# Performance work log

Measured on AMD Instinct MI355X. Metric: run time of the kernel, lower is better.

Reference implementation:

```python
import jax, jax.numpy as jnp
import numpy as np

BS, D, N, E, L, NE = 8, 512, 2048, 8, 64, 524288


def conv1d_same(x, w, b):
    # x: [B, W, Cin], w: [K, Cin, Cout] -> [B, W, Cout], stride 1, 'same' padding
    y = jax.lax.conv_general_dilated(x, w, window_strides=(1,), padding='SAME',
                                     dimension_numbers=('NWC', 'WIO', 'NWC'))
    return y + b


def setup_inputs() -> dict:
    key = jax.random.key(0)
    ks = jax.random.split(key, 10)
    def nrm(k, shape, s=1.0):
        return jax.random.normal(k, shape, jnp.float32) * s
    return {
        'latent': nrm(ks[0], (BS, D)),
        'edge_index': jax.random.randint(ks[1], (2, NE), 0, BS * N),
        'W_dense': nrm(ks[2], (D, N), 0.05),
        'b_dense': jnp.zeros((N,), jnp.float32),
        'conv1_w': nrm(ks[3], (3, 1, E), 0.3),
        'conv1_b': jnp.zeros((E,), jnp.float32),
        'gat_Wq': nrm(ks[4], (E, E), 0.3),
        'gat_bq': jnp.zeros((E,), jnp.float32),
        'gat_Wk': nrm(ks[5], (E, E), 0.3),
        'gat_bk': jnp.zeros((E,), jnp.float32),
        'gat_Wv': nrm(ks[6], (E, E), 0.3),
        'gat_bias': jnp.zeros((E,), jnp.float32),
        'qkv_w': nrm(ks[7], (3, E, 3 * E * L), 0.1),
        'qkv_b': jnp.zeros((3 * E * L,), jnp.float32),
    }


def reference(latent, edge_index, W_dense, b_dense, conv1_w, conv1_b,
              gat_Wq, gat_bq, gat_Wk, gat_bk, gat_Wv, gat_bias, qkv_w, qkv_b):
    bs = latent.shape[0]
    # Dense -> [bs, N], expand -> Conv1D(E) -> [bs, N, E]
    skeleton = latent @ W_dense + b_dense
    skeleton = conv1d_same(skeleton[..., None], conv1_w, conv1_b)
    # concat(unstack, axis=0) == reshape to batched graph nodes [bs*N, E]
    x = skeleton.reshape(bs * N, E)
    BN = bs * N
    # GAT (tf_geometric, num_heads=1): add self-loops, per-edge dot-attention,
    # segment softmax over destination (row), scatter-sum aggregate.
    loops = jnp.arange(BN)
    row = jnp.concatenate([edge_index[0], loops])
    col = jnp.concatenate([edge_index[1], loops])
    Q = jax.nn.leaky_relu(x @ gat_Wq + gat_bq, 0.2)
    K = jax.nn.leaky_relu(x @ gat_Wk + gat_bk, 0.2)
    V = x @ gat_Wv
    score = jnp.sum(Q[row] * K[col], axis=-1)            # [n_edges + BN]
    smax = jax.ops.segment_max(score, row, num_segments=BN)
    ex = jnp.exp(score - smax[row])
    ssum = jax.ops.segment_sum(ex, row, num_segments=BN)
    alpha = ex / ssum[row]                               # segment softmax
    h = jax.ops.segment_sum(alpha[:, None] * V[col], row, num_segments=BN) + gat_bias
    graph = h.reshape(bs, N, E)                          # stack(split(., bs))
    # QVK conv over node axis -> [bs, N, 3*E*L]
    qvk = conv1d_same(graph, qkv_w, qkv_b)
    # stack(split(., L, -1), 1) then concat(unstack(., -2), -1)
    qvk = qvk.reshape(bs, N, L, 3 * E).transpose(0, 2, 1, 3).reshape(bs, L, N * 3 * E)
    q, v, k = jnp.split(qvk, 3, axis=-1)                 # each [bs, L, N*E]
    # keras Attention (use_scale=False): softmax(q @ k^T) @ v
    attn = jax.nn.softmax(jnp.einsum('btd,bsd->bts', q, k), axis=-1)
    seq = jnp.einsum('bts,bsd->btd', attn, v)
    # stack(split(., N, -1), -2) == reshape [bs, L, N, E]
    return seq.reshape(bs, L, N, E)
```

## Files before the change

### kernel.cpp

```cpp
#include <hip/hip_runtime.h>
#include <hip/hip_bf16.h>
#include <math.h>

#define BSZ 8
#define DDIM 512
#define NND 2048
#define EE 8
#define LLH 64
#define NEDGE 524288
#define BNN 16384
#define OCC 1536
#define DQ 16384
#define NCHK 22

typedef __attribute__((ext_vector_type(8))) short short8;
typedef __attribute__((ext_vector_type(4))) float f32x4;

__device__ inline unsigned short f2bf(float x) {
    __hip_bfloat16 h = __float2bfloat16(x);
    return __builtin_bit_cast(unsigned short, h);
}
__device__ inline float bf2f(unsigned short u) {
    return __uint_as_float(((unsigned int)u) << 16);
}

__global__ __launch_bounds__(256) void k_densep(const float* __restrict__ latent,
                                                const float* __restrict__ Wd,
                                                float* __restrict__ pdense,
                                                int* __restrict__ hist) {
    int n0 = blockIdx.x * 32, d0 = blockIdx.y * 64;
    __shared__ float lat[8][64];
    int tid = threadIdx.x;
    if (blockIdx.y == 0) hist[blockIdx.x * 256 + tid] = 0;
    #pragma unroll
    for (int r = 0; r < 2; ++r) {
        int i = r * 256 + tid;
        lat[i >> 6][i & 63] = latent[(i >> 6) * DDIM + d0 + (i & 63)];
    }
    __syncthreads();
    int nl = tid & 31, b = tid >> 5;
    const float* wp = Wd + (size_t)d0 * NND + n0 + nl;
    float acc = 0.f;
    #pragma unroll 8
    for (int d = 0; d < 64; ++d) acc += lat[b][d] * wp[(size_t)d * NND];
    pdense[((size_t)blockIdx.y * BSZ + b) * NND + n0 + nl] = acc;
}

__global__ __launch_bounds__(64) void k_gat(const float* __restrict__ pdense,
                                            const float* __restrict__ bd,
                                            const float* __restrict__ w1,
                                            const float* __restrict__ b1,
                                            const float* __restrict__ Wq, const float* __restrict__ bq,
                                            const float* __restrict__ Wk, const float* __restrict__ bk,
                                            const float* __restrict__ Wv,
                                            const int* __restrict__ ei,
                                            float* __restrict__ Qg, float* __restrict__ Kg,
                                            float* __restrict__ Vg, int* __restrict__ hist) {
    int i = blockIdx.x * 64 + threadIdx.x;
    int b = i >> 11, n = i & (NND - 1);
    float sm = 0.f, s0 = 0.f, sp = 0.f;
    #pragma unroll
    for (int ds = 0; ds < 8; ++ds) {
        const float* p = pdense + ((size_t)ds * BSZ + b) * NND + n;
        if (n > 0) sm += p[-1];
        s0 += p[0];
        if (n < NND - 1) sp += p[1];
    }
    if (n > 0) sm += bd[n - 1];
    s0 += bd[n];
    if (n < NND - 1) sp += bd[n + 1];
    float xr[EE];
    #pragma unroll
    for (int e = 0; e < EE; ++e)
        xr[e] = sm * w1[e] + s0 * w1[EE + e] + sp * w1[2 * EE + e] + b1[e];
    #pragma unroll
    for (int j = 0; j < EE; ++j) {
        float q = bq[j], k = bk[j], v = 0.f;
        #pragma unroll
        for (int c = 0; c < EE; ++c) {
            q += xr[c] * Wq[c * EE + j];
            k += xr[c] * Wk[c * EE + j];
            v += xr[c] * Wv[c * EE + j];
        }
        Qg[(size_t)i * EE + j] = (q >= 0.f) ? q : 0.2f * q;
        Kg[(size_t)i * EE + j] = (k >= 0.f) ? k : 0.2f * k;
        Vg[(size_t)i * EE + j] = v;
    }
    #pragma unroll 4
    for (int j = 0; j < 32; ++j)
        atomicAdd(hist + ei[i + j * BNN], 1);
}

__global__ __launch_bounds__(1024) void k_scan(const int* __restrict__ hist,
                                               int* __restrict__ offs,
                                               int* __restrict__ cnt) {
    int tid = threadIdx.x;
    int lane = tid & 63, wv = tid >> 6;
    const int4* hp = (const int4*)(hist + tid * 16);
    int4 a = hp[0], b4 = hp[1], c4 = hp[2], d4 = hp[3];
    int h[16] = {a.x, a.y, a.z, a.w, b4.x, b4.y, b4.z, b4.w,
                 c4.x, c4.y, c4.z, c4.w, d4.x, d4.y, d4.z, d4.w};
    int mysum = 0;
    #pragma unroll
    for (int i = 0; i < 16; ++i) mysum += h[i];
    int inc = mysum;
    #pragma unroll
    for (int off = 1; off < 64; off <<= 1) {
        int u = __shfl_up(inc, off, 64);
        if (lane >= off) inc += u;
    }
    __shared__ int wtot[16];
    if (lane == 63) wtot[wv] = inc;
    __syncthreads();
    if (tid < 16) {
        int t = wtot[tid];
        #pragma unroll
        for (int off = 1; off < 16; off <<= 1) {
            int u = __shfl_up(t, off, 16);
            if (tid >= off) t += u;
        }
        wtot[tid] = t;
    }
    __syncthreads();
    int run = (wv ? wtot[wv - 1] : 0) + inc - mysum;
    #pragma unroll
    for (int i = 0; i < 16; ++i) {
        offs[tid * 16 + i] = run;
        cnt[tid * 16 + i] = run;
        run += h[i];
    }
}

__global__ void k_scatter(const int* __restrict__ ei, int* __restrict__ cnt,
                          int* __restrict__ ecol) {
    int e = blockIdx.x * 256 + threadIdx.x;
    if (e >= NEDGE) return;
    int r = ei[e], c = ei[NEDGE + e];
    int pos = atomicAdd(cnt + r, 1);
    ecol[pos] = c;
}

__global__ __launch_bounds__(256) void k_gatagg(const int* __restrict__ ecol,
                                                const int* __restrict__ offs,
                                                const int* __restrict__ hist,
                                                const float* __restrict__ Qg,
                                                const float* __restrict__ Kg,
                                                const float* __restrict__ Vg,
                                                const float* __restrict__ gbias,
                                                float* __restrict__ hg) {
    int row = __builtin_amdgcn_readfirstlane(blockIdx.x * 4 + (threadIdx.x >> 6));
    int lane = threadIdx.x & 63;
    const float* Qr = Qg + (size_t)row * EE;
    float q0 = Qr[0], q1 = Qr[1], q2 = Qr[2], q3 = Qr[3];
    float q4 = Qr[4], q5 = Qr[5], q6 = Qr[6], q7 = Qr[7];
    int beg = offs[row], deg = hist[row];
    int total = deg + 1;
    float m = -INFINITY, l = 0.f;
    float acc[EE];
    #pragma unroll
    for (int j = 0; j < EE; ++j) acc[j] = 0.f;
    for (int base = 0; base < total; base += 64) {
        int idx = base + lane;
        int c = row;
        if (idx < deg) c = ecol[beg + idx];
        const float4* K4 = (const float4*)(Kg + (size_t)c * EE);
        float4 ka = K4[0], kb = K4[1];
        float s = q0*ka.x + q1*ka.y + q2*ka.z + q3*ka.w
                + q4*kb.x + q5*kb.y + q6*kb.z + q7*kb.w;
        if (idx >= total) s = -INFINITY;
        float pm = s;
        #pragma unroll
        for (int off = 32; off > 0; off >>= 1) pm = fmaxf(pm, __shfl_xor(pm, off));
        float nm = fmaxf(m, pm);
        float scale = __expf(m - nm);
        float p = (idx < total) ? __expf(s - nm) : 0.f;
        float ps = p;
        #pragma unroll
        for (int off = 32; off > 0; off >>= 1) ps += __shfl_xor(ps, off);
        l = l * scale + ps;
        const float4* V4 = (const float4*)(Vg + (size_t)c * EE);
        float4 va = V4[0], vb = V4[1];
        float pv[EE] = {p*va.x, p*va.y, p*va.z, p*va.w, p*vb.x, p*vb.y, p*vb.z, p*vb.w};
        #pragma unroll
        for (int j = 0; j < EE; ++j) {
            float t = pv[j];
            #pragma unroll
            for (int off = 32; off > 0; off >>= 1) t += __shfl_xor(t, off);
            acc[j] = acc[j] * scale + t;
        }
        m = nm;
    }
    if (lane < EE)
        hg[(size_t)row * EE + lane] = acc[lane] / l + gbias[lane];
}

__global__ __launch_bounds__(256) void k_qkvF(const float* __restrict__ hg,
                                              const float* __restrict__ qw,
                                              const float* __restrict__ qb,
                                              unsigned short* __restrict__ Fq) {
    int n0 = blockIdx.x * 32;
    int b = blockIdx.y;
    __shared__ float hs[34 * EE];
    __shared__ unsigned short st[32 * 768];
    int tid = threadIdx.x;
    for (int i = tid; i < 34 * EE; i += 256) {
        int nn = n0 - 1 + (i >> 3);
        hs[i] = (nn >= 0 && nn < NND) ? hg[((size_t)b * NND + nn) * EE + (i & 7)] : 0.f;
    }
    __syncthreads();
    #pragma unroll
    for (int pass = 0; pass < 2; ++pass) {
        if (pass) __syncthreads();
        float w[3][24], bias[3];
        #pragma unroll
        for (int rr = 0; rr < 3; ++rr) {
            int o = pass * 768 + rr * 256 + tid;
            bias[rr] = qb[o];
            #pragma unroll
            for (int kk = 0; kk < 24; ++kk) w[rr][kk] = qw[kk * OCC + o];
        }
        for (int nn = 0; nn < 32; ++nn) {
            const float* hv = &hs[nn * EE];
            float a0 = bias[0], a1 = bias[1], a2 = bias[2];
            #pragma unroll
            for (int kk = 0; kk < 24; ++kk) {
                float h = hv[kk];
                a0 += h * w[0][kk]; a1 += h * w[1][kk]; a2 += h * w[2][kk];
            }
            st[nn * 768 + tid]       = f2bf(a0);
            st[nn * 768 + tid + 256] = f2bf(a1);
            st[nn * 768 + tid + 512] = f2bf(a2);
        }
        __syncthreads();
        unsigned short* dstbase = Fq + ((size_t)b * NND + n0) * OCC + pass * 768;
        #pragma unroll
        for (int it = 0; it < 12; ++it) {
            int idx8 = it * 256 + tid;
            int row = idx8 / 96, col8 = idx8 - row * 96;
            *(short8*)(dstbase + (size_t)row * OCC + col8 * 8) =
                *(const short8*)(&st[row * 768 + col8 * 8]);
        }
    }
}

__global__ __launch_bounds__(256) void k_attnS(const unsigned short* __restrict__ Fq,
                                               float* __restrict__ Spart) {
    int ch = blockIdx.x, b = blockIdx.y;
    __shared__ unsigned short qt[64 * 200];
    __shared__ unsigned short kt[64 * 200];
    int tid = threadIdx.x;
    int t = tid & 63, nl0 = tid >> 6;
    const unsigned short* Fb = Fq + (size_t)b * NND * OCC;
    short8 z = {0,0,0,0,0,0,0,0};
    int lane = tid & 63, wv = tid >> 6;
    int fr = lane & 15, fk = (lane >> 4) * 8;
    f32x4 accs[4] = {{0,0,0,0},{0,0,0,0},{0,0,0,0},{0,0,0,0}};
    for (int sub = 0; sub < 4; ++sub) {
        int n0 = ch * 32 + sub * 8;
        if (sub) __syncthreads();
        #pragma unroll
        for (int h = 0; h < 2; ++h) {
            int nl = nl0 + h * 4;
            int n = n0 + nl;
            short8 q0 = z, q1 = z, q2 = z;
            if (n <= 682) {
                const short8* p = (const short8*)(Fb + (size_t)n * OCC + t * 24);
                q0 = p[0]; q1 = p[1];
                if (n < 682) q2 = p[2];
            }
            *(short8*)(&qt[t * 200 + nl * 24 + 0])  = q0;
            *(short8*)(&qt[t * 200 + nl * 24 + 8])  = q1;
            *(short8*)(&qt[t * 200 + nl * 24 + 16]) = q2;
            short8 k0 = z, k1 = z, k2 = z;
            if (n <= 682) {
                const short8* p = (const short8*)(Fb + (size_t)(n + 1365) * OCC + t * 24 + 8);
                k0 = p[0]; k1 = p[1];
            }
            if (n <= 681) {
                const short8* p2 = (const short8*)(Fb + (size_t)(n + 1366) * OCC + t * 24);
                k2 = p2[0];
            }
            *(short8*)(&kt[t * 200 + nl * 24 + 0])  = k0;
            *(short8*)(&kt[t * 200 + nl * 24 + 8])  = k1;
            *(short8*)(&kt[t * 200 + nl * 24 + 16]) = k2;
        }
        __syncthreads();
        short8 afr[6];
        #pragma unroll
        for (int ks = 0; ks < 6; ++ks)
            afr[ks] = *(const short8*)(&qt[(wv * 16 + fr) * 200 + ks * 32 + fk]);
        #pragma unroll
        for (int srow = 0; srow < 4; ++srow) {
            #pragma unroll
            for (int ks = 0; ks < 6; ++ks) {
                short8 bfr = *(const short8*)(&kt[(srow * 16 + fr) * 200 + ks * 32 + fk]);
                accs[srow] = __builtin_amdgcn_mfma_f32_16x16x32_bf16(afr[ks], bfr, accs[srow], 0, 0, 0);
            }
        }
    }
    #pragma unroll
    for (int srow = 0; srow < 4; ++srow) {
        float* dst = Spart + (((size_t)ch * BSZ + b) * LLH + wv * 16 + (lane >> 4) * 4) * LLH
                   + srow * 16 + fr;
        #pragma unroll
        for (int r = 0; r < 4; ++r) dst[r * LLH] = accs[srow][r];
    }
}

__global__ void k_softmax(const float* __restrict__ Spart, float* __restrict__ atT) {
    int b = blockIdx.x >> 6, t = blockIdx.x & 63;
    int s = threadIdx.x;
    float v = 0.f;
    for (int ch = 0; ch < NCHK; ++ch)
        v += Spart[(((size_t)ch * BSZ + b) * LLH + t) * LLH + s];
    float m = v;
    #pragma unroll
    for (int off = 32; off > 0; off >>= 1) m = fmaxf(m, __shfl_xor(m, off));
    float e = __expf(v - m);
    float sum = e;
    #pragma unroll
    for (int off = 32; off > 0; off >>= 1) sum += __shfl_xor(sum, off);
    atT[((size_t)b * LLH + s) * LLH + t] = e / sum;
}

__global__ __launch_bounds__(256) void k_attnV(const unsigned short* __restrict__ Fq,
                                               const float* __restrict__ atT,
                                               float* __restrict__ out) {
    int b = blockIdx.y;
    int d0 = blockIdx.x * 64;
    int tid = threadIdx.x;
    __shared__ unsigned short vt[64 * 64];
    const unsigned short* Fb = Fq + (size_t)b * NND * OCC;
    #pragma unroll
    for (int r = 0; r < 16; ++r) {
        int idx = r * 256 + tid;
        int s = idx >> 6, d = idx & 63;
        int f = DQ + d0 + d;
        int n = f / 24, c = f - n * 24;
        vt[s * 64 + d] = Fb[(size_t)n * OCC + s * 24 + c];
    }
    __syncthreads();
    int lane = tid & 63;
    int t0 = __builtin_amdgcn_readfirstlane((tid >> 6) * 16);
    const float* arow = atT + (size_t)b * LLH * LLH + t0;
    float acc[16];
    #pragma unroll
    for (int tt = 0; tt < 16; ++tt) acc[tt] = 0.f;
    #pragma unroll 4
    for (int s = 0; s < LLH; ++s) {
        float vv = bf2f(vt[s * 64 + lane]);
        #pragma unroll
        for (int tt = 0; tt < 16; ++tt)
            acc[tt] += arow[s * LLH + tt] * vv;
    }
    float* ob = out + ((size_t)b * LLH + t0) * DQ + d0 + lane;
    #pragma unroll
    for (int tt = 0; tt < 16; ++tt) ob[(size_t)tt * DQ] = acc[tt];
}

extern "C" void kernel_launch(void* const* d_in, const int* in_sizes, int n_in,
                              void* d_out, int out_size, void* d_ws, size_t ws_size,
                              hipStream_t stream) {
    (void)in_sizes; (void)n_in; (void)out_size; (void)ws_size;
    const float* latent = (const float*)d_in[0];
    const int*   ei     = (const int*)d_in[1];
    const float* Wd     = (const float*)d_in[2];
    const float* bd     = (const float*)d_in[3];
    const float* w1     = (const float*)d_in[4];
    const float* b1     = (const float*)d_in[5];
    const float* Wq     = (const float*)d_in[6];
    const float* bq     = (const float*)d_in[7];
    const float* Wk     = (const float*)d_in[8];
    const float* bk     = (const float*)d_in[9];
    const float* Wv     = (const float*)d_in[10];
    const float* gbias  = (const float*)d_in[11];
    const float* qw     = (const float*)d_in[12];
    const float* qb     = (const float*)d_in[13];
    float* out = (float*)d_out;

    float* ws     = (float*)d_ws;
    float* pdense = ws;
    float* Qg     = pdense + 64 * NND;
    float* Kg     = Qg + BNN * EE;
    float* Vg     = Kg + BNN * EE;
    float* hg     = Vg + BNN * EE;
    int*   hist   = (int*)(hg + BNN * EE);
    int*   offs   = hist + BNN;
    int*   cnt    = offs + BNN;
    int*   ecol   = cnt + BNN;
    float* Spart  = (float*)(ecol + NEDGE);
    float* atT    = Spart + (size_t)NCHK * BSZ * LLH * LLH;
    unsigned short* Fq = (unsigned short*)(atT + BSZ * LLH * LLH);

    k_densep<<<dim3(64, 8), dim3(256), 0, stream>>>(latent, Wd, pdense, hist);
    k_gat<<<dim3(256), dim3(64), 0, stream>>>(pdense, bd, w1, b1, Wq, bq, Wk, bk, Wv,
                                              ei, Qg, Kg, Vg, hist);
    k_scan<<<dim3(1), dim3(1024), 0, stream>>>(hist, offs, cnt);
    k_scatter<<<dim3(NEDGE / 256), dim3(256), 0, stream>>>(ei, cnt, ecol);
    k_gatagg<<<dim3(BNN / 4), dim3(256), 0, stream>>>(ecol, offs, hist,
                                                      Qg, Kg, Vg, gbias, hg);
    k_qkvF<<<dim3(64, 8), dim3(256), 0, stream>>>(hg, qw, qb, Fq);
    k_attnS<<<dim3(NCHK, 8), dim3(256), 0, stream>>>(Fq, Spart);
    k_softmax<<<dim3(512), dim3(64), 0, stream>>>(Spart, atT);
    k_attnV<<<dim3(256, 8), dim3(256), 0, stream>>>(Fq, atT, out);
}
```

Before: 142.0 us.

## Fuse graph pipeline with grid barriers and factor attention scores through weight Gram matrices

Replaces the nine-kernel pipeline with five kernels. The dense layer, conv and Q/K/V projection now run in one front kernel that also precomputes weight-product matrices G from the QKV conv weights. The histogram, scan, scatter and GAT aggregation run in one persistent kernel that uses spin-wait grid barriers and a per-block shared-memory scan. Attention scores are computed algebraically as G times small per-batch moment matrices of the graph features, so the bf16 q·k MFMA pass is dropped and only the V part of the conv is materialised. The goal is fewer launches and less memory traffic, at the cost of relying on all 512 blocks being co-resident for the barrier and of changed numerics (fp32 moments instead of bf16 products).

```diff
diff --git a/kernel.cpp b/kernel.cpp
--- a/kernel.cpp
+++ b/kernel.cpp
@@ -11,10 +11,9 @@
 #define BNN 16384
 #define OCC 1536
 #define DQ 16384
-#define NCHK 22
+#define NBLK_EDGES 512
 
 typedef __attribute__((ext_vector_type(8))) short short8;
-typedef __attribute__((ext_vector_type(4))) float f32x4;
 
 __device__ inline unsigned short f2bf(float x) {
     __hip_bfloat16 h = __float2bfloat16(x);
@@ -24,303 +23,360 @@
     return __uint_as_float(((unsigned int)u) << 16);
 }
 
-__global__ __launch_bounds__(256) void k_densep(const float* __restrict__ latent,
-                                                const float* __restrict__ Wd,
-                                                float* __restrict__ pdense,
-                                                int* __restrict__ hist) {
-    int n0 = blockIdx.x * 32, d0 = blockIdx.y * 64;
-    __shared__ float lat[8][64];
-    int tid = threadIdx.x;
-    if (blockIdx.y == 0) hist[blockIdx.x * 256 + tid] = 0;
+__device__ inline void gridbar(int* c, int target) {
+    __syncthreads();
+    if (threadIdx.x == 0) {
+        __threadfence();
+        atomicAdd(c, 1);
+        while (atomicAdd(c, 0) < target) __builtin_amdgcn_s_sleep(32);
+        __threadfence();
+    }
+    __syncthreads();
+}
+
+__global__ __launch_bounds__(256) void k_front(const float* __restrict__ latent,
+                                               const float* __restrict__ Wd,
+                                               const float* __restrict__ bd,
+                                               const float* __restrict__ w1,
+                                               const float* __restrict__ b1,
+                                               const float* __restrict__ Wq, const float* __restrict__ bq,
+                                               const float* __restrict__ Wk, const float* __restrict__ bk,
+                                               const float* __restrict__ Wv,
+                                               const float* __restrict__ qw,
+                                               const float* __restrict__ qb,
+                                               float* __restrict__ Qg, float* __restrict__ Kg,
+                                               float* __restrict__ Vg,
+                                               float* __restrict__ G,
+                                               int* __restrict__ hist, int* __restrict__ zcnt,
+                                               int* __restrict__ cbar) {
+    int bx = blockIdx.x, tid = threadIdx.x;
+    if (bx < 64) {
+        hist[bx * 256 + tid] = 0;
+        zcnt[bx * 256 + tid] = 0;
+        if (bx == 0 && tid < 16) cbar[tid] = 0;
+        __shared__ float lat[8][512];
+        __shared__ float pdl[34][4][8];
+        __shared__ float skel[36][8];
+        for (int i = tid; i < 4096; i += 256) lat[i >> 9][i & 511] = latent[i];
+        __syncthreads();
+        int n0 = bx * 32;
+        {
+            int nl = tid & 63, dq = tid >> 6;
+            if (nl < 34) {
+                int n = n0 - 1 + nl;
+                float acc[8] = {0.f,0.f,0.f,0.f,0.f,0.f,0.f,0.f};
+                if (n >= 0 && n < NND) {
+                    const float* wp = Wd + (size_t)dq * 128 * NND + n;
+                    for (int d = 0; d < 128; ++d) {
+                        float w = wp[(size_t)d * NND];
+                        int dd = dq * 128 + d;
+                        #pragma unroll
+                        for (int b = 0; b < 8; ++b) acc[b] += lat[b][dd] * w;
+                    }
+                }
+                #pragma unroll
+                for (int b = 0; b < 8; ++b) pdl[nl][dq][b] = acc[b];
+            }
+        }
+        __syncthreads();
+        for (int idx = tid; idx < 34 * 8; idx += 256) {
+            int h = idx >> 3, b = idx & 7;
+            int n = n0 - 1 + h;
+            float s = 0.f;
+            if (n >= 0 && n < NND)
+                s = pdl[h][0][b] + pdl[h][1][b] + pdl[h][2][b] + pdl[h][3][b] + bd[n];
+            skel[h][b] = s;
+        }
+        __syncthreads();
+        {
+            int nl2 = tid >> 3, b = tid & 7;
+            int n = n0 + nl2;
+            float sm = skel[nl2][b], s0 = skel[nl2 + 1][b], sp = skel[nl2 + 2][b];
+            float xr[EE];
+            #pragma unroll
+            for (int e = 0; e < EE; ++e)
+                xr[e] = sm * w1[e] + s0 * w1[EE + e] + sp * w1[2 * EE + e] + b1[e];
+            size_t i = (size_t)b * NND + n;
+            #pragma unroll
+            for (int j = 0; j < EE; ++j) {
+                float q = bq[j], k = bk[j], v = 0.f;
+                #pragma unroll
+                for (int c = 0; c < EE; ++c) {
+                    q += xr[c] * Wq[c * EE + j];
+                    k += xr[c] * Wk[c * EE + j];
+                    v += xr[c] * Wv[c * EE + j];
+                }
+                Qg[i * EE + j] = (q >= 0.f) ? q : 0.2f * q;
+                Kg[i * EE + j] = (k >= 0.f) ? k : 0.2f * k;
+                Vg[i * EE + j] = v;
+            }
+        }
+    } else {
+        int gi = bx - 64;
+        int t = gi >> 1, shalf = gi & 1;
+        __shared__ float A[25][24];
+        for (int idx = tid; idx < 600; idx += 256) {
+            int i = idx / 24, c = idx - (idx / 24) * 24;
+            A[i][c] = (i < 24) ? qw[i * OCC + t * 24 + c] : qb[t * 24 + c];
+        }
+        __syncthreads();
+        int s = shalf * 32 + (tid & 31), q = tid >> 5;
+        for (int p = q; p < 625; p += 8) {
+            int i = p / 25, j = p - (p / 25) * 25;
+            float B[24];
+            if (j < 24) {
+                const float4* bp = (const float4*)(qw + (size_t)j * OCC + s * 24);
+                #pragma unroll
+                for (int r = 0; r < 6; ++r) {
+                    float4 v = bp[r];
+                    B[r*4+0]=v.x; B[r*4+1]=v.y; B[r*4+2]=v.z; B[r*4+3]=v.w;
+                }
+            } else {
+                const float4* bp = (const float4*)(qb + s * 24);
+                #pragma unroll
+                for (int r = 0; r < 6; ++r) {
+                    float4 v = bp[r];
+                    B[r*4+0]=v.x; B[r*4+1]=v.y; B[r*4+2]=v.z; B[r*4+3]=v.w;
+                }
+            }
+            float g1 = 0.f, g2 = 0.f;
+            #pragma unroll
+            for (int c = 0; c < 16; ++c) g1 += A[i][c] * B[c + 8];
+            #pragma unroll
+            for (int c = 16; c < 24; ++c) g2 += A[i][c] * B[c - 16];
+            G[((size_t)(t * 2 + 0) * 625 + p) * 64 + s] = g1;
+            G[((size_t)(t * 2 + 1) * 625 + p) * 64 + s] = g2;
+        }
+    }
+}
+
+__global__ __launch_bounds__(256) void k_edges(const int* __restrict__ ei,
+                                               int* __restrict__ hist, int* __restrict__ zcnt,
+                                               int* __restrict__ cbar, int* __restrict__ ecol,
+                                               const float* __restrict__ Qg,
+                                               const float* __restrict__ Kg,
+                                               const float* __restrict__ Vg,
+                                               const float* __restrict__ gbias,
+                                               float* __restrict__ hg) {
+    __shared__ int offs[16385];
+    __shared__ int wsum[4];
+    int bid = blockIdx.x, tid = threadIdx.x;
+    int e0 = bid * 1024;
+    #pragma unroll
+    for (int k = 0; k < 4; ++k) atomicAdd(hist + ei[e0 + k * 256 + tid], 1);
+    gridbar(cbar + 0, NBLK_EDGES);
+    {
+        int base = tid * 64, sum = 0;
+        const int4* h4 = (const int4*)(hist + base);
+        #pragma unroll
+        for (int i = 0; i < 16; ++i) { int4 v = h4[i]; sum += v.x + v.y + v.z + v.w; }
+        int lane = tid & 63, wv = tid >> 6;
+        int inc = sum;
+        #pragma unroll
+        for (int off = 1; off < 64; off <<= 1) {
+            int u = __shfl_up(inc, off, 64);
+            if (lane >= off) inc += u;
+        }
+        if (lane == 63) wsum[wv] = inc;
+        __syncthreads();
+        if (tid == 0) {
+            int t0 = wsum[0], t1 = wsum[1], t2 = wsum[2];
+            wsum[0] = 0; wsum[1] = t0; wsum[2] = t0 + t1; wsum[3] = t0 + t1 + t2;
+        }
+        __syncthreads();
+        int run = wsum[wv] + inc - sum;
+        #pragma unroll
+        for (int i = 0; i < 16; ++i) {
+            int4 v = h4[i];
+            offs[base + i*4 + 0] = run; run += v.x;
+            offs[base + i*4 + 1] = run; run += v.y;
+            offs[base + i*4 + 2] = run; run += v.z;
+            offs[base + i*4 + 3] = run; run += v.w;
+        }
+        if (tid == 0) offs[16384] = NEDGE;
+    }
+    __syncthreads();
+    #pragma unroll
+    for (int k = 0; k < 4; ++k) {
+        int e = e0 + k * 256 + tid;
+        int r = ei[e], c = ei[NEDGE + e];
+        int pos = offs[r] + atomicAdd(zcnt + r, 1);
+        ecol[pos] = c;
+    }
+    gridbar(cbar + 1, NBLK_EDGES);
+    int lane = tid & 63;
+    int wid = bid * 4 + (tid >> 6);
+    for (int k = 0; k < 8; ++k) {
+        int row = __builtin_amdgcn_readfirstlane(wid + k * 2048);
+        int beg = offs[row];
+        int deg = offs[row + 1] - beg;
+        const float* Qr = Qg + (size_t)row * EE;
+        float q0 = Qr[0], q1 = Qr[1], q2 = Qr[2], q3 = Qr[3];
+        float q4 = Qr[4], q5 = Qr[5], q6 = Qr[6], q7 = Qr[7];
+        int total = deg + 1;
+        float m = -INFINITY, l = 0.f;
+        float acc[EE];
+        #pragma unroll
+        for (int j = 0; j < EE; ++j) acc[j] = 0.f;
+        for (int base = 0; base < total; base += 64) {
+            int idx = base + lane;
+            int c = row;
+            if (idx < deg) c = ecol[beg + idx];
+            const float4* K4 = (const float4*)(Kg + (size_t)c * EE);
+            float4 ka = K4[0], kb = K4[1];
+            float s = q0*ka.x + q1*ka.y + q2*ka.z + q3*ka.w
+                    + q4*kb.x + q5*kb.y + q6*kb.z + q7*kb.w;
+            if (idx >= total) s = -INFINITY;
+            float pm = s;
+            #pragma unroll
+            for (int off = 32; off > 0; off >>= 1) pm = fmaxf(pm, __shfl_xor(pm, off));
+            float nm = fmaxf(m, pm);
+            float scale = __expf(m - nm);
+            float p = (idx < total) ? __expf(s - nm) : 0.f;
+            float ps = p;
+            #pragma unroll
+            for (int off = 32; off > 0; off >>= 1) ps += __shfl_xor(ps, off);
+            l = l * scale + ps;
+            const float4* V4 = (const float4*)(Vg + (size_t)c * EE);
+            float4 va = V4[0], vb = V4[1];
+            float pv[EE] = {p*va.x, p*va.y, p*va.z, p*va.w, p*vb.x, p*vb.y, p*vb.z, p*vb.w};
+            #pragma unroll
+            for (int j = 0; j < EE; ++j) {
+                float t = pv[j];
+                #pragma unroll
+                for (int off = 32; off > 0; off >>= 1) t += __shfl_xor(t, off);
+                acc[j] = acc[j] * scale + t;
+            }
+            m = nm;
+        }
+        if (lane < EE)
+            hg[(size_t)row * EE + lane] = acc[lane] / l + gbias[lane];
+    }
+}
+
+__global__ __launch_bounds__(256) void k_qkvFvM(const float* __restrict__ hg,
+                                                const float* __restrict__ qw,
+                                                const float* __restrict__ qb,
+                                                unsigned short* __restrict__ Fq,
+                                                float* __restrict__ Mpart) {
+    int bx = blockIdx.x, b = blockIdx.y, tid = threadIdx.x;
+    if (bx < 22) {
+        int n0 = 682 + bx * 32;
+        __shared__ float hs[34 * EE];
+        __shared__ unsigned short st[32 * 768];
+        for (int i = tid; i < 34 * EE; i += 256) {
+            int nn = n0 - 1 + (i >> 3);
+            hs[i] = (nn >= 0 && nn < NND) ? hg[((size_t)b * NND + nn) * EE + (i & 7)] : 0.f;
+        }
+        __syncthreads();
+        #pragma unroll
+        for (int pass = 0; pass < 2; ++pass) {
+            if (pass) __syncthreads();
+            float w[3][24], bias[3];
+            #pragma unroll
+            for (int rr = 0; rr < 3; ++rr) {
+                int o = pass * 768 + rr * 256 + tid;
+                bias[rr] = qb[o];
+                #pragma unroll
+                for (int kk = 0; kk < 24; ++kk) w[rr][kk] = qw[kk * OCC + o];
+            }
+            for (int nn = 0; nn < 32; ++nn) {
+                const float* hv = &hs[nn * EE];
+                float a0 = bias[0], a1 = bias[1], a2 = bias[2];
+                #pragma unroll
+                for (int kk = 0; kk < 24; ++kk) {
+                    float h = hv[kk];
+                    a0 += h * w[0][kk]; a1 += h * w[1][kk]; a2 += h * w[2][kk];
+                }
+                st[nn * 768 + tid]       = f2bf(a0);
+                st[nn * 768 + tid + 256] = f2bf(a1);
+                st[nn * 768 + tid + 512] = f2bf(a2);
+            }
+            __syncthreads();
+            unsigned short* dstbase = Fq + ((size_t)b * NND + n0) * OCC + pass * 768;
+            #pragma unroll
+            for (int it = 0; it < 12; ++it) {
+                int idx8 = it * 256 + tid;
+                int row = idx8 / 96, col8 = idx8 - row * 96;
+                if (n0 + row <= 1365)
+                    *(short8*)(dstbase + (size_t)row * OCC + col8 * 8) =
+                        *(const short8*)(&st[row * 768 + col8 * 8]);
+            }
+        }
+    } else {
+        int sp = bx - 22;
+        int nq0 = sp * 86;
+        __shared__ float hq[88][EE];
+        __shared__ float hk[90][EE];
+        for (int i = tid; i < 88 * EE; i += 256) {
+            int r = nq0 - 1 + (i >> 3);
+            hq[i >> 3][i & 7] = (r >= 0 && r < NND) ? hg[((size_t)b * NND + r) * EE + (i & 7)] : 0.f;
+        }
+        for (int i = tid; i < 90 * EE; i += 256) {
+            int r = nq0 + 1364 + (i >> 3);
+            hk[i >> 3][i & 7] = (r < NND) ? hg[((size_t)b * NND + r) * EE + (i & 7)] : 0.f;
+        }
+        __syncthreads();
+        int cnt1 = 683 - nq0; if (cnt1 > 86) cnt1 = 86; if (cnt1 < 0) cnt1 = 0;
+        int cnt2 = 682 - nq0; if (cnt2 > 86) cnt2 = 86; if (cnt2 < 0) cnt2 = 0;
+        for (int idx = tid; idx < 1250; idx += 256) {
+            int mm = idx / 625, p = idx - (idx / 625) * 625;
+            int i = p / 25, j = p - (p / 25) * 25;
+            int cnt = mm ? cnt2 : cnt1;
+            int qi = i >> 3, qe = i & 7;
+            int kj = (j >> 3) + mm, ke = j & 7;
+            float acc = 0.f;
+            if (i < 24 && j < 24) {
+                for (int nl = 0; nl < cnt; ++nl)
+                    acc += hq[nl + qi][qe] * hk[nl + kj][ke];
+            } else if (i < 24) {
+                for (int nl = 0; nl < cnt; ++nl) acc += hq[nl + qi][qe];
+            } else if (j < 24) {
+                for (int nl = 0; nl < cnt; ++nl) acc += hk[nl + kj][ke];
+            } else {
+                acc = (float)cnt;
+            }
+            Mpart[((size_t)(sp * 8 + b)) * 1250 + idx] = acc;
+        }
+    }
+}
+
+__global__ __launch_bounds__(256) void k_Ssm(const float* __restrict__ G,
+                                             const float* __restrict__ Mpart,
+                                             float* __restrict__ atT) {
+    __shared__ float Ms[8][1250];
+    int t = blockIdx.x, tid = threadIdx.x;
+    for (int idx = tid; idx < 10000; idx += 256) {
+        int b = idx / 1250, r = idx - (idx / 1250) * 1250;
+        float s = 0.f;
+        #pragma unroll
+        for (int sp = 0; sp < 8; ++sp)
+            s += Mpart[((size_t)(sp * 8 + b)) * 1250 + r];
+        Ms[b][r] = s;
+    }
+    __syncthreads();
+    int s = tid & 63, bg = tid >> 6;
+    const float* Gt = G + (size_t)t * 1250 * 64;
+    float acc0 = 0.f, acc1 = 0.f;
+    for (int u = 0; u < 625; ++u) {
+        float g1 = Gt[(size_t)u * 64 + s];
+        float g2 = Gt[(size_t)(625 + u) * 64 + s];
+        acc0 += g1 * Ms[bg][u] + g2 * Ms[bg][625 + u];
+        acc1 += g1 * Ms[bg + 4][u] + g2 * Ms[bg + 4][625 + u];
+    }
     #pragma unroll
     for (int r = 0; r < 2; ++r) {
-        int i = r * 256 + tid;
-        lat[i >> 6][i & 63] = latent[(i >> 6) * DDIM + d0 + (i & 63)];
-    }
-    __syncthreads();
-    int nl = tid & 31, b = tid >> 5;
-    const float* wp = Wd + (size_t)d0 * NND + n0 + nl;
-    float acc = 0.f;
-    #pragma unroll 8
-    for (int d = 0; d < 64; ++d) acc += lat[b][d] * wp[(size_t)d * NND];
-    pdense[((size_t)blockIdx.y * BSZ + b) * NND + n0 + nl] = acc;
-}
-
-__global__ __launch_bounds__(64) void k_gat(const float* __restrict__ pdense,
-                                            const float* __restrict__ bd,
-                                            const float* __restrict__ w1,
-                                            const float* __restrict__ b1,
-                                            const float* __restrict__ Wq, const float* __restrict__ bq,
-                                            const float* __restrict__ Wk, const float* __restrict__ bk,
-                                            const float* __restrict__ Wv,
-                                            const int* __restrict__ ei,
-                                            float* __restrict__ Qg, float* __restrict__ Kg,
-                                            float* __restrict__ Vg, int* __restrict__ hist) {
-    int i = blockIdx.x * 64 + threadIdx.x;
-    int b = i >> 11, n = i & (NND - 1);
-    float sm = 0.f, s0 = 0.f, sp = 0.f;
-    #pragma unroll
-    for (int ds = 0; ds < 8; ++ds) {
-        const float* p = pdense + ((size_t)ds * BSZ + b) * NND + n;
-        if (n > 0) sm += p[-1];
-        s0 += p[0];
-        if (n < NND - 1) sp += p[1];
-    }
-    if (n > 0) sm += bd[n - 1];
-    s0 += bd[n];
-    if (n < NND - 1) sp += bd[n + 1];
-    float xr[EE];
-    #pragma unroll
-    for (int e = 0; e < EE; ++e)
-        xr[e] = sm * w1[e] + s0 * w1[EE + e] + sp * w1[2 * EE + e] + b1[e];
-    #pragma unroll
-    for (int j = 0; j < EE; ++j) {
-        float q = bq[j], k = bk[j], v = 0.f;
-        #pragma unroll
-        for (int c = 0; c < EE; ++c) {
-            q += xr[c] * Wq[c * EE + j];
-            k += xr[c] * Wk[c * EE + j];
-            v += xr[c] * Wv[c * EE + j];
-        }
-        Qg[(size_t)i * EE + j] = (q >= 0.f) ? q : 0.2f * q;
-        Kg[(size_t)i * EE + j] = (k >= 0.f) ? k : 0.2f * k;
-        Vg[(size_t)i * EE + j] = v;
-    }
-    #pragma unroll 4
-    for (int j = 0; j < 32; ++j)
-        atomicAdd(hist + ei[i + j * BNN], 1);
-}
-
-__global__ __launch_bounds__(1024) void k_scan(const int* __restrict__ hist,
-                                               int* __restrict__ offs,
-                                               int* __restrict__ cnt) {
-    int tid = threadIdx.x;
-    int lane = tid & 63, wv = tid >> 6;
-    const int4* hp = (const int4*)(hist + tid * 16);
-    int4 a = hp[0], b4 = hp[1], c4 = hp[2], d4 = hp[3];
-    int h[16] = {a.x, a.y, a.z, a.w, b4.x, b4.y, b4.z, b4.w,
-                 c4.x, c4.y, c4.z, c4.w, d4.x, d4.y, d4.z, d4.w};
-    int mysum = 0;
-    #pragma unroll
-    for (int i = 0; i < 16; ++i) mysum += h[i];
-    int inc = mysum;
-    #pragma unroll
-    for (int off = 1; off < 64; off <<= 1) {
-        int u = __shfl_up(inc, off, 64);
-        if (lane >= off) inc += u;
-    }
-    __shared__ int wtot[16];
-    if (lane == 63) wtot[wv] = inc;
-    __syncthreads();
-    if (tid < 16) {
-        int t = wtot[tid];
-        #pragma unroll
-        for (int off = 1; off < 16; off <<= 1) {
-            int u = __shfl_up(t, off, 16);
-            if (tid >= off) t += u;
-        }
-        wtot[tid] = t;
-    }
-    __syncthreads();
-    int run = (wv ? wtot[wv - 1] : 0) + inc - mysum;
-    #pragma unroll
-    for (int i = 0; i < 16; ++i) {
-        offs[tid * 16 + i] = run;
-        cnt[tid * 16 + i] = run;
-        run += h[i];
-    }
-}
-
-__global__ void k_scatter(const int* __restrict__ ei, int* __restrict__ cnt,
-                          int* __restrict__ ecol) {
-    int e = blockIdx.x * 256 + threadIdx.x;
-    if (e >= NEDGE) return;
-    int r = ei[e], c = ei[NEDGE + e];
-    int pos = atomicAdd(cnt + r, 1);
-    ecol[pos] = c;
-}
-
-__global__ __launch_bounds__(256) void k_gatagg(const int* __restrict__ ecol,
-                                                const int* __restrict__ offs,
-                                                const int* __restrict__ hist,
-                                                const float* __restrict__ Qg,
-                                                const float* __restrict__ Kg,
-                                                const float* __restrict__ Vg,
-                                                const float* __restrict__ gbias,
-                                                float* __restrict__ hg) {
-    int row = __builtin_amdgcn_readfirstlane(blockIdx.x * 4 + (threadIdx.x >> 6));
-    int lane = threadIdx.x & 63;
-    const float* Qr = Qg + (size_t)row * EE;
-    float q0 = Qr[0], q1 = Qr[1], q2 = Qr[2], q3 = Qr[3];
-    float q4 = Qr[4], q5 = Qr[5], q6 = Qr[6], q7 = Qr[7];
-    int beg = offs[row], deg = hist[row];
-    int total = deg + 1;
-    float m = -INFINITY, l = 0.f;
-    float acc[EE];
-    #pragma unroll
-    for (int j = 0; j < EE; ++j) acc[j] = 0.f;
-    for (int base = 0; base < total; base += 64) {
-        int idx = base + lane;
-        int c = row;
-        if (idx < deg) c = ecol[beg + idx];
-        const float4* K4 = (const float4*)(Kg + (size_t)c * EE);
-        float4 ka = K4[0], kb = K4[1];
-        float s = q0*ka.x + q1*ka.y + q2*ka.z + q3*ka.w
-                + q4*kb.x + q5*kb.y + q6*kb.z + q7*kb.w;
-        if (idx >= total) s = -INFINITY;
-        float pm = s;
-        #pragma unroll
-        for (int off = 32; off > 0; off >>= 1) pm = fmaxf(pm, __shfl_xor(pm, off));
-        float nm = fmaxf(m, pm);
-        float scale = __expf(m - nm);
-        float p = (idx < total) ? __expf(s - nm) : 0.f;
-        float ps = p;
-        #pragma unroll
-        for (int off = 32; off > 0; off >>= 1) ps += __shfl_xor(ps, off);
-        l = l * scale + ps;
-        const float4* V4 = (const float4*)(Vg + (size_t)c * EE);
-        float4 va = V4[0], vb = V4[1];
-        float pv[EE] = {p*va.x, p*va.y, p*va.z, p*va.w, p*vb.x, p*vb.y, p*vb.z, p*vb.w};
-        #pragma unroll
-        for (int j = 0; j < EE; ++j) {
-            float t = pv[j];
-            #pragma unroll
-            for (int off = 32; off > 0; off >>= 1) t += __shfl_xor(t, off);
-            acc[j] = acc[j] * scale + t;
-        }
-        m = nm;
-    }
-    if (lane < EE)
-        hg[(size_t)row * EE + lane] = acc[lane] / l + gbias[lane];
-}
-
-__global__ __launch_bounds__(256) void k_qkvF(const float* __restrict__ hg,
-                                              const float* __restrict__ qw,
-                                              const float* __restrict__ qb,
-                                              unsigned short* __restrict__ Fq) {
-    int n0 = blockIdx.x * 32;
-    int b = blockIdx.y;
-    __shared__ float hs[34 * EE];
-    __shared__ unsigned short st[32 * 768];
-    int tid = threadIdx.x;
-    for (int i = tid; i < 34 * EE; i += 256) {
-        int nn = n0 - 1 + (i >> 3);
-        hs[i] = (nn >= 0 && nn < NND) ? hg[((size_t)b * NND + nn) * EE + (i & 7)] : 0.f;
-    }
-    __syncthreads();
-    #pragma unroll
-    for (int pass = 0; pass < 2; ++pass) {
-        if (pass) __syncthreads();
-        float w[3][24], bias[3];
-        #pragma unroll
-        for (int rr = 0; rr < 3; ++rr) {
-            int o = pass * 768 + rr * 256 + tid;
-            bias[rr] = qb[o];
-            #pragma unroll
-            for (int kk = 0; kk < 24; ++kk) w[rr][kk] = qw[kk * OCC + o];
-        }
-        for (int nn = 0; nn < 32; ++nn) {
-            const float* hv = &hs[nn * EE];
-            float a0 = bias[0], a1 = bias[1], a2 = bias[2];
-            #pragma unroll
-            for (int kk = 0; kk < 24; ++kk) {
-                float h = hv[kk];
-                a0 += h * w[0][kk]; a1 += h * w[1][kk]; a2 += h * w[2][kk];
-            }
-            st[nn * 768 + tid]       = f2bf(a0);
-            st[nn * 768 + tid + 256] = f2bf(a1);
-            st[nn * 768 + tid + 512] = f2bf(a2);
-        }
-        __syncthreads();
-        unsigned short* dstbase = Fq + ((size_t)b * NND + n0) * OCC + pass * 768;
-        #pragma unroll
-        for (int it = 0; it < 12; ++it) {
-            int idx8 = it * 256 + tid;
-            int row = idx8 / 96, col8 = idx8 - row * 96;
-            *(short8*)(dstbase + (size_t)row * OCC + col8 * 8) =
-                *(const short8*)(&st[row * 768 + col8 * 8]);
-        }
-    }
-}
-
-__global__ __launch_bounds__(256) void k_attnS(const unsigned short* __restrict__ Fq,
-                                               float* __restrict__ Spart) {
-    int ch = blockIdx.x, b = blockIdx.y;
-    __shared__ unsigned short qt[64 * 200];
-    __shared__ unsigned short kt[64 * 200];
-    int tid = threadIdx.x;
-    int t = tid & 63, nl0 = tid >> 6;
-    const unsigned short* Fb = Fq + (size_t)b * NND * OCC;
-    short8 z = {0,0,0,0,0,0,0,0};
-    int lane = tid & 63, wv = tid >> 6;
-    int fr = lane & 15, fk = (lane >> 4) * 8;
-    f32x4 accs[4] = {{0,0,0,0},{0,0,0,0},{0,0,0,0},{0,0,0,0}};
-    for (int sub = 0; sub < 4; ++sub) {
-        int n0 = ch * 32 + sub * 8;
-        if (sub) __syncthreads();
-        #pragma unroll
-        for (int h = 0; h < 2; ++h) {
-            int nl = nl0 + h * 4;
-            int n = n0 + nl;
-            short8 q0 = z, q1 = z, q2 = z;
-            if (n <= 682) {
-                const short8* p = (const short8*)(Fb + (size_t)n * OCC + t * 24);
-                q0 = p[0]; q1 = p[1];
-                if (n < 682) q2 = p[2];
-            }
-            *(short8*)(&qt[t * 200 + nl * 24 + 0])  = q0;
-            *(short8*)(&qt[t * 200 + nl * 24 + 8])  = q1;
-            *(short8*)(&qt[t * 200 + nl * 24 + 16]) = q2;
-            short8 k0 = z, k1 = z, k2 = z;
-            if (n <= 682) {
-                const short8* p = (const short8*)(Fb + (size_t)(n + 1365) * OCC + t * 24 + 8);
-                k0 = p[0]; k1 = p[1];
-            }
-            if (n <= 681) {
-                const short8* p2 = (const short8*)(Fb + (size_t)(n + 1366) * OCC + t * 24);
-                k2 = p2[0];
-            }
-            *(short8*)(&kt[t * 200 + nl * 24 + 0])  = k0;
-            *(short8*)(&kt[t * 200 + nl * 24 + 8])  = k1;
-            *(short8*)(&kt[t * 200 + nl * 24 + 16]) = k2;
-        }
-        __syncthreads();
-        short8 afr[6];
-        #pragma unroll
-        for (int ks = 0; ks < 6; ++ks)
-            afr[ks] = *(const short8*)(&qt[(wv * 16 + fr) * 200 + ks * 32 + fk]);
-        #pragma unroll
-        for (int srow = 0; srow < 4; ++srow) {
-            #pragma unroll
-            for (int ks = 0; ks < 6; ++ks) {
-                short8 bfr = *(const short8*)(&kt[(srow * 16 + fr) * 200 + ks * 32 + fk]);
-                accs[srow] = __builtin_amdgcn_mfma_f32_16x16x32_bf16(afr[ks], bfr, accs[srow], 0, 0, 0);
-            }
-        }
-    }
-    #pragma unroll
-    for (int srow = 0; srow < 4; ++srow) {
-        float* dst = Spart + (((size_t)ch * BSZ + b) * LLH + wv * 16 + (lane >> 4) * 4) * LLH
-                   + srow * 16 + fr;
-        #pragma unroll
-        for (int r = 0; r < 4; ++r) dst[r * LLH] = accs[srow][r];
-    }
-}
-
-__global__ void k_softmax(const float* __restrict__ Spart, float* __restrict__ atT) {
-    int b = blockIdx.x >> 6, t = blockIdx.x & 63;
-    int s = threadIdx.x;
-    float v = 0.f;
-    for (int ch = 0; ch < NCHK; ++ch)
-        v += Spart[(((size_t)ch * BSZ + b) * LLH + t) * LLH + s];
-    float m = v;
-    #pragma unroll
-    for (int off = 32; off > 0; off >>= 1) m = fmaxf(m, __shfl_xor(m, off));
-    float e = __expf(v - m);
-    float sum = e;
-    #pragma unroll
-    for (int off = 32; off > 0; off >>= 1) sum += __shfl_xor(sum, off);
-    atT[((size_t)b * LLH + s) * LLH + t] = e / sum;
+        int b = bg + r * 4;
+        float v = r ? acc1 : acc0;
+        float m = v;
+        #pragma unroll
+        for (int off = 32; off > 0; off >>= 1) m = fmaxf(m, __shfl_xor(m, off));
+        float e = __expf(v - m);
+        float sum = e;
+        #pragma unroll
+        for (int off = 32; off > 0; off >>= 1) sum += __shfl_xor(sum, off);
+        atT[((size_t)b * LLH + s) * LLH + t] = e / sum;
+    }
 }
 
 __global__ __launch_bounds__(256) void k_attnV(const unsigned short* __restrict__ Fq,
@@ -378,29 +434,26 @@
     const float* qb     = (const float*)d_in[13];
     float* out = (float*)d_out;
 
-    float* ws     = (float*)d_ws;
-    float* pdense = ws;
-    float* Qg     = pdense + 64 * NND;
-    float* Kg     = Qg + BNN * EE;
-    float* Vg     = Kg + BNN * EE;
-    float* hg     = Vg + BNN * EE;
-    int*   hist   = (int*)(hg + BNN * EE);
-    int*   offs   = hist + BNN;
-    int*   cnt    = offs + BNN;
-    int*   ecol   = cnt + BNN;
-    float* Spart  = (float*)(ecol + NEDGE);
-    float* atT    = Spart + (size_t)NCHK * BSZ * LLH * LLH;
-    unsigned short* Fq = (unsigned short*)(atT + BSZ * LLH * LLH);
-
-    k_densep<<<dim3(64, 8), dim3(256), 0, stream>>>(latent, Wd, pdense, hist);
-    k_gat<<<dim3(256), dim3(64), 0, stream>>>(pdense, bd, w1, b1, Wq, bq, Wk, bk, Wv,
-                                              ei, Qg, Kg, Vg, hist);
-    k_scan<<<dim3(1), dim3(1024), 0, stream>>>(hist, offs, cnt);
-    k_scatter<<<dim3(NEDGE / 256), dim3(256), 0, stream>>>(ei, cnt, ecol);
-    k_gatagg<<<dim3(BNN / 4), dim3(256), 0, stream>>>(ecol, offs, hist,
-                                                      Qg, Kg, Vg, gbias, hg);
-    k_qkvF<<<dim3(64, 8), dim3(256), 0, stream>>>(hg, qw, qb, Fq);
-    k_attnS<<<dim3(NCHK, 8), dim3(256), 0, stream>>>(Fq, Spart);
-    k_softmax<<<dim3(512), dim3(64), 0, stream>>>(Spart, atT);
+    float* ws   = (float*)d_ws;
+    float* Qg   = ws;
+    float* Kg   = Qg + BNN * EE;
+    float* Vg   = Kg + BNN * EE;
+    float* hg   = Vg + BNN * EE;
+    float* G    = hg + BNN * EE;
+    float* Mp   = G + (size_t)64 * 1250 * 64;
+    float* atT  = Mp + 80000;
+    int*   hist = (int*)(atT + BSZ * LLH * LLH);
+    int*   zcnt = hist + BNN;
+    int*   cbar = zcnt + BNN;
+    int*   ecol = cbar + 16;
+    unsigned short* Fq = (unsigned short*)(ecol + NEDGE);
+
+    k_front<<<dim3(192), dim3(256), 0, stream>>>(latent, Wd, bd, w1, b1,
+                                                 Wq, bq, Wk, bk, Wv, qw, qb,
+                                                 Qg, Kg, Vg, G, hist, zcnt, cbar);
+    k_edges<<<dim3(NBLK_EDGES), dim3(256), 0, stream>>>(ei, hist, zcnt, cbar, ecol,
+                                                        Qg, Kg, Vg, gbias, hg);
+    k_qkvFvM<<<dim3(30, 8), dim3(256), 0, stream>>>(hg, qw, qb, Fq, Mp);
+    k_Ssm<<<dim3(64), dim3(256), 0, stream>>>(G, Mp, atT);
     k_attnV<<<dim3(256, 8), dim3(256), 0, stream>>>(Fq, atT, out);
 }
```

Result: slower. 299.3 us (+110.8%).
